# Performance work log

Hardware: AMD Instinct MI355X
Metric: run time of the kernel (lower is better)

Reference implementation:

```python
import jax, jax.numpy as jnp
import numpy as np
from jax import lax

S = 9      # patch feature size (3x3 flattened)
HID = 15   # MI-net hidden width
B = 4096
IMG = 192
PAD = 6


def _linear_params(k, fin, fout):
    bound = 1.0 / np.sqrt(fin)
    kw, kb = jax.random.split(k)
    w = jax.random.uniform(kw, (fout, fin), minval=-bound, maxval=bound, dtype=jnp.float32)
    b = jax.random.uniform(kb, (fout,), minval=-bound, maxval=bound, dtype=jnp.float32)
    return w, b


def setup_inputs() -> dict:
    key = jax.random.key(0)
    ks = jax.random.split(key, 12)
    x = jax.random.normal(ks[0], (B, 1, IMG, IMG), dtype=jnp.float32)
    hc = IMG // 3  # conv output side (stride-3 valid conv)
    ij = jax.random.randint(ks[1], (B, 2), 0, hc, dtype=jnp.int32)
    perm = jax.random.permutation(ks[2], B).astype(jnp.int32)
    cb = 1.0 / np.sqrt(1 * 3 * 3)
    conv_w = jax.random.uniform(ks[3], (1, 1, 3, 3), minval=-cb, maxval=cb, dtype=jnp.float32)
    conv_b = jax.random.uniform(ks[4], (1,), minval=-cb, maxval=cb, dtype=jnp.float32)
    xw1, xb1 = _linear_params(ks[5], S, S)
    xw2, xb2 = _linear_params(ks[6], S, S)
    xw3, xb3 = _linear_params(ks[7], S, HID)
    yw1, yb1 = _linear_params(ks[8], S, S)
    yw2, yb2 = _linear_params(ks[9], S, S)
    yw3, yb3 = _linear_params(ks[10], S, HID)
    fw, fb = _linear_params(ks[11], HID, 1)
    return dict(x=x, ij=ij, perm=perm, conv_w=conv_w, conv_b=conv_b,
                xw1=xw1, xb1=xb1, xw2=xw2, xb2=xb2, xw3=xw3, xb3=xb3,
                yw1=yw1, yb1=yb1, yw2=yw2, yb2=yb2, yw3=yw3, yb3=yb3,
                fw=fw, fb=fb)


def _mi_net(p1, p2, xw1, xb1, xw2, xb2, xw3, xb3,
            yw1, yb1, yw2, yb2, yw3, yb3, fw, fb):
    ix = p1 + jax.nn.relu(p1 @ xw1.T + xb1)
    ix = ix + jax.nn.relu(ix @ xw2.T + xb2)
    ix = ix @ xw3.T + xb3
    iy = p2 + jax.nn.relu(p2 @ yw1.T + yb1)
    iy = iy + jax.nn.relu(iy @ yw2.T + yb2)
    iy = iy @ yw3.T + yb3
    h1 = jax.nn.relu(ix + iy)
    return h1 @ fw.T + fb  # [B, 1]


def reference(x, ij, perm, conv_w, conv_b,
              xw1, xb1, xw2, xb2, xw3, xb3,
              yw1, yb1, yw2, yb2, yw3, yb3, fw, fb):
    # stride-3 valid conv: [B,1,IMG,IMG] -> [B,1,64,64]
    co = lax.conv_general_dilated(x, conv_w, (3, 3), 'VALID',
                                  dimension_numbers=('NCHW', 'OIHW', 'NCHW'))
    co = co[:, 0] + conv_b[0]  # [B, Hc, Wc]
    bn, hc, wc = co.shape
    # pad_circular(data, 6)[i:i+3, j:j+6] == data[(i-6+r) % Hc, (j-6+c) % Wc]
    rows = (ij[:, 0:1] - PAD + jnp.arange(3, dtype=jnp.int32)) % hc  # [B,3]
    cols = (ij[:, 1:2] - PAD + jnp.arange(6, dtype=jnp.int32)) % wc  # [B,6]
    rect = co[jnp.arange(bn)[:, None, None], rows[:, :, None], cols[:, None, :]]  # [B,3,6]
    patch1 = rect[:, :, :3].reshape(-1, S)
    patch2 = rect[:, :, 3:].reshape(-1, S)
    patch2_sh = patch2[perm]
    pred_xy = _mi_net(patch1, patch2, xw1, xb1, xw2, xb2, xw3, xb3,
                      yw1, yb1, yw2, yb2, yw3, yb3, fw, fb)
    pred_x_y = _mi_net(patch1, patch2_sh, xw1, xb1, xw2, xb2, xw3, xb3,
                       yw1, yb1, yw2, yb2, yw3, yb3, fw, fb)
    ret = jnp.mean(pred_xy) - jnp.log(jnp.mean(jnp.exp(pred_x_y)))
    return -ret
```

## Files before the change

### kernel.cpp

```cpp
#include <hip/hip_runtime.h>
#include <math.h>

#define BATCH 4096
#define IMGD 192
#define HC 64
#define PADV 6
#define NBLK 64
#define ITEMS 64

__device__ __forceinline__ void branch9(const float* __restrict__ s, int off,
                                        const float* __restrict__ p, float* __restrict__ out)
{
    float v[9];
    #pragma unroll
    for (int j = 0; j < 9; ++j) {
        float a = s[off + 81 + j];
        #pragma unroll
        for (int k = 0; k < 9; ++k) a += p[k] * s[off + j * 9 + k];
        v[j] = p[j] + fmaxf(a, 0.0f);
    }
    float u[9];
    #pragma unroll
    for (int j = 0; j < 9; ++j) {
        float a = s[off + 171 + j];
        #pragma unroll
        for (int k = 0; k < 9; ++k) a += v[k] * s[off + 90 + j * 9 + k];
        u[j] = v[j] + fmaxf(a, 0.0f);
    }
    #pragma unroll
    for (int j = 0; j < 15; ++j) {
        float a = s[off + 315 + j];
        #pragma unroll
        for (int k = 0; k < 9; ++k) a += u[k] * s[off + 180 + j * 9 + k];
        out[j] = a;
    }
}

__global__ __launch_bounds__(256) void k_fused(
    const float* __restrict__ x, const int* __restrict__ ij,
    const int* __restrict__ perm,
    const float* __restrict__ cw, const float* __restrict__ cb,
    const float* __restrict__ xw1, const float* __restrict__ xb1,
    const float* __restrict__ xw2, const float* __restrict__ xb2,
    const float* __restrict__ xw3, const float* __restrict__ xb3,
    const float* __restrict__ yw1, const float* __restrict__ yb1,
    const float* __restrict__ yw2, const float* __restrict__ yb2,
    const float* __restrict__ yw3, const float* __restrict__ yb3,
    const float* __restrict__ fw, const float* __restrict__ fb,
    float* __restrict__ partials)
{
    __shared__ float s[676];
    __shared__ float lpatch[ITEMS * 27];
    __shared__ float bout[192 * 15];

    int t = threadIdx.x;

    for (int i = t; i < 81; i += 256)  { s[i] = xw1[i];        s[330 + i] = yw1[i];
                                         s[90 + i] = xw2[i];   s[420 + i] = yw2[i]; }
    for (int i = t; i < 135; i += 256) { s[180 + i] = xw3[i];  s[510 + i] = yw3[i]; }
    if (t < 9)  { s[81 + t] = xb1[t];   s[171 + t] = xb2[t];
                  s[411 + t] = yb1[t];  s[501 + t] = yb2[t]; }
    if (t < 15) { s[315 + t] = xb3[t];  s[645 + t] = yb3[t];  s[660 + t] = fw[t]; }
    if (t == 0) s[675] = fb[0];

    float w[9];
    #pragma unroll
    for (int i = 0; i < 9; ++i) w[i] = cw[i];
    float cbias = cb[0];

    int b0 = blockIdx.x * ITEMS;

    for (int idx = t; idx < ITEMS * 27; idx += 256) {
        int item = idx / 27;
        int p    = idx - item * 27;
        int bb, r, c, slot;
        if (p < 18) {
            bb = b0 + item;
            r = p / 6;  c = p - r * 6;
            int half = (c >= 3) ? 1 : 0;
            slot = half * 9 + r * 3 + (c - 3 * half);
        } else {
            int q = p - 18;
            bb = perm[b0 + item];
            r = q / 3;  c = 3 + (q - r * 3);
            slot = 18 + q;
        }
        int i0 = ij[2 * bb], j0 = ij[2 * bb + 1];
        int rr = i0 - PADV + r;  if (rr < 0) rr += HC;
        int cc = j0 - PADV + c;  if (cc < 0) cc += HC;
        const float* xp = x + (size_t)bb * (IMGD * IMGD)
                            + (size_t)(rr * 3) * IMGD + cc * 3;
        float v = cbias;
        v += xp[0]          * w[0] + xp[1]            * w[1] + xp[2]            * w[2];
        v += xp[IMGD]       * w[3] + xp[IMGD + 1]     * w[4] + xp[IMGD + 2]     * w[5];
        v += xp[2 * IMGD]   * w[6] + xp[2 * IMGD + 1] * w[7] + xp[2 * IMGD + 2] * w[8];
        lpatch[item * 27 + slot] = v;
    }
    __syncthreads();

    if (t < 192) {
        int item   = t & 63;
        int branch = t >> 6;
        int woff   = (branch == 0) ? 0 : 330;
        int pbase  = item * 27 + branch * 9;
        float p[9];
        #pragma unroll
        for (int k = 0; k < 9; ++k) p[k] = lpatch[pbase + k];
        float o[15];
        branch9(s, woff, p, o);
        #pragma unroll
        for (int j = 0; j < 15; ++j) bout[t * 15 + j] = o[j];
    }
    __syncthreads();

    if (t < 64) {
        float fbv = s[675];
        float pxy = fbv, pxs = fbv;
        #pragma unroll
        for (int j = 0; j < 15; ++j) {
            float oxj  = bout[t * 15 + j];
            float oyj  = bout[(64 + t) * 15 + j];
            float oysj = bout[(128 + t) * 15 + j];
            float fwj  = s[660 + j];
            pxy += fmaxf(oxj + oyj,  0.0f) * fwj;
            pxs += fmaxf(oxj + oysj, 0.0f) * fwj;
        }
        float e = expf(pxs);
        #pragma unroll
        for (int o = 32; o > 0; o >>= 1) {
            pxy += __shfl_down(pxy, o);
            e   += __shfl_down(e, o);
        }
        if (t == 0) {
            partials[blockIdx.x]        = pxy;
            partials[NBLK + blockIdx.x] = e;
        }
    }
}

__global__ __launch_bounds__(64) void k_final(const float* __restrict__ partials,
                                              float* __restrict__ out)
{
    int t = threadIdx.x;
    float sx = partials[t];
    float se = partials[NBLK + t];
    #pragma unroll
    for (int o = 32; o > 0; o >>= 1) {
        sx += __shfl_down(sx, o);
        se += __shfl_down(se, o);
    }
    if (t == 0) out[0] = logf(se / (float)BATCH) - sx / (float)BATCH;
}

extern "C" void kernel_launch(void* const* d_in, const int* in_sizes, int n_in,
                              void* d_out, int out_size, void* d_ws, size_t ws_size,
                              hipStream_t stream)
{
    const float* x    = (const float*)d_in[0];
    const int*   ij   = (const int*)d_in[1];
    const int*   perm = (const int*)d_in[2];
    const float* cw   = (const float*)d_in[3];
    const float* cb   = (const float*)d_in[4];
    const float* xw1  = (const float*)d_in[5];
    const float* xb1  = (const float*)d_in[6];
    const float* xw2  = (const float*)d_in[7];
    const float* xb2  = (const float*)d_in[8];
    const float* xw3  = (const float*)d_in[9];
    const float* xb3  = (const float*)d_in[10];
    const float* yw1  = (const float*)d_in[11];
    const float* yb1  = (const float*)d_in[12];
    const float* yw2  = (const float*)d_in[13];
    const float* yb2  = (const float*)d_in[14];
    const float* yw3  = (const float*)d_in[15];
    const float* yb3  = (const float*)d_in[16];
    const float* fw   = (const float*)d_in[17];
    const float* fb   = (const float*)d_in[18];

    float* partials = (float*)d_ws;

    k_fused<<<NBLK, 256, 0, stream>>>(x, ij, perm, cw, cb,
                                      xw1, xb1, xw2, xb2, xw3, xb3,
                                      yw1, yb1, yw2, yb2, yw3, yb3,
                                      fw, fb, partials);
    k_final<<<1, 64, 0, stream>>>(partials, (float*)d_out);
}
```

Before: 14.57 us.

## Spread batch over 256 blocks of 16 items and stage perm/ij indices in LDS

Raises the grid from 64 to 256 blocks, each handling 16 batch items instead of 64, so more CUs on the GPU get work. The perm and ij lookups are loaded once per item into shared memory in two dependent stages, so the dependent global reads no longer repeat per patch element. The final reduction kernel now combines 256 partials across four wavefronts. The cost is two extra block barriers, and only 48 of 256 threads run the MLP stage.

```diff
diff --git a/kernel.cpp b/kernel.cpp
--- a/kernel.cpp
+++ b/kernel.cpp
@@ -5,8 +5,8 @@
 #define IMGD 192
 #define HC 64
 #define PADV 6
-#define NBLK 64
-#define ITEMS 64
+#define NBLK2 256
+#define IPB 16
 
 __device__ __forceinline__ void branch9(const float* __restrict__ s, int off,
                                         const float* __restrict__ p, float* __restrict__ out)
@@ -50,10 +50,13 @@
     float* __restrict__ partials)
 {
     __shared__ float s[676];
-    __shared__ float lpatch[ITEMS * 27];
-    __shared__ float bout[192 * 15];
-
-    int t = threadIdx.x;
+    __shared__ int   pidx[IPB];
+    __shared__ int   ij4[IPB * 4];
+    __shared__ float lpatch[IPB * 27];
+    __shared__ float bout[48 * 15];
+
+    int t  = threadIdx.x;
+    int b0 = blockIdx.x * IPB;
 
     for (int i = t; i < 81; i += 256)  { s[i] = xw1[i];        s[330 + i] = yw1[i];
                                          s[90 + i] = xw2[i];   s[420 + i] = yw2[i]; }
@@ -68,24 +71,32 @@
     for (int i = 0; i < 9; ++i) w[i] = cw[i];
     float cbias = cb[0];
 
-    int b0 = blockIdx.x * ITEMS;
-
-    for (int idx = t; idx < ITEMS * 27; idx += 256) {
+    if (t < IPB) pidx[t] = perm[b0 + t];
+    __syncthreads();
+    if (t < 2 * IPB) {
+        int item = t & (IPB - 1);
+        int sel  = t >> 4;
+        int bb   = sel ? pidx[item] : (b0 + item);
+        ij4[item * 4 + sel * 2 + 0] = ij[2 * bb];
+        ij4[item * 4 + sel * 2 + 1] = ij[2 * bb + 1];
+    }
+    __syncthreads();
+
+    for (int idx = t; idx < IPB * 27; idx += 256) {
         int item = idx / 27;
         int p    = idx - item * 27;
-        int bb, r, c, slot;
+        int r, c, sel, slot;
         if (p < 18) {
-            bb = b0 + item;
-            r = p / 6;  c = p - r * 6;
+            r = p / 6;  c = p - r * 6;  sel = 0;
             int half = (c >= 3) ? 1 : 0;
             slot = half * 9 + r * 3 + (c - 3 * half);
         } else {
             int q = p - 18;
-            bb = perm[b0 + item];
-            r = q / 3;  c = 3 + (q - r * 3);
+            r = q / 3;  c = 3 + (q - r * 3);  sel = 1;
             slot = 18 + q;
         }
-        int i0 = ij[2 * bb], j0 = ij[2 * bb + 1];
+        int bb = sel ? pidx[item] : (b0 + item);
+        int i0 = ij4[item * 4 + sel * 2], j0 = ij4[item * 4 + sel * 2 + 1];
         int rr = i0 - PADV + r;  if (rr < 0) rr += HC;
         int cc = j0 - PADV + c;  if (cc < 0) cc += HC;
         const float* xp = x + (size_t)bb * (IMGD * IMGD)
@@ -98,9 +109,9 @@
     }
     __syncthreads();
 
-    if (t < 192) {
-        int item   = t & 63;
-        int branch = t >> 6;
+    if (t < 48) {
+        int item   = t & 15;
+        int branch = t >> 4;
         int woff   = (branch == 0) ? 0 : 330;
         int pbase  = item * 27 + branch * 9;
         float p[9];
@@ -113,43 +124,51 @@
     }
     __syncthreads();
 
-    if (t < 64) {
+    if (t < IPB) {
         float fbv = s[675];
         float pxy = fbv, pxs = fbv;
         #pragma unroll
         for (int j = 0; j < 15; ++j) {
             float oxj  = bout[t * 15 + j];
-            float oyj  = bout[(64 + t) * 15 + j];
-            float oysj = bout[(128 + t) * 15 + j];
+            float oyj  = bout[(16 + t) * 15 + j];
+            float oysj = bout[(32 + t) * 15 + j];
             float fwj  = s[660 + j];
             pxy += fmaxf(oxj + oyj,  0.0f) * fwj;
             pxs += fmaxf(oxj + oysj, 0.0f) * fwj;
         }
         float e = expf(pxs);
         #pragma unroll
-        for (int o = 32; o > 0; o >>= 1) {
+        for (int o = 8; o > 0; o >>= 1) {
             pxy += __shfl_down(pxy, o);
             e   += __shfl_down(e, o);
         }
         if (t == 0) {
-            partials[blockIdx.x]        = pxy;
-            partials[NBLK + blockIdx.x] = e;
-        }
-    }
-}
-
-__global__ __launch_bounds__(64) void k_final(const float* __restrict__ partials,
-                                              float* __restrict__ out)
-{
+            partials[blockIdx.x]         = pxy;
+            partials[NBLK2 + blockIdx.x] = e;
+        }
+    }
+}
+
+__global__ __launch_bounds__(256) void k_final(const float* __restrict__ partials,
+                                               float* __restrict__ out)
+{
+    __shared__ float r1[4], r2[4];
     int t = threadIdx.x;
     float sx = partials[t];
-    float se = partials[NBLK + t];
+    float se = partials[NBLK2 + t];
     #pragma unroll
     for (int o = 32; o > 0; o >>= 1) {
         sx += __shfl_down(sx, o);
         se += __shfl_down(se, o);
     }
-    if (t == 0) out[0] = logf(se / (float)BATCH) - sx / (float)BATCH;
+    int wid = t >> 6, lane = t & 63;
+    if (lane == 0) { r1[wid] = sx; r2[wid] = se; }
+    __syncthreads();
+    if (t == 0) {
+        float S  = (r1[0] + r1[1]) + (r1[2] + r1[3]);
+        float E  = (r2[0] + r2[1]) + (r2[2] + r2[3]);
+        out[0] = logf(E / (float)BATCH) - S / (float)BATCH;
+    }
 }
 
 extern "C" void kernel_launch(void* const* d_in, const int* in_sizes, int n_in,
@@ -178,9 +197,9 @@
 
     float* partials = (float*)d_ws;
 
-    k_fused<<<NBLK, 256, 0, stream>>>(x, ij, perm, cw, cb,
-                                      xw1, xb1, xw2, xb2, xw3, xb3,
-                                      yw1, yb1, yw2, yb2, yw3, yb3,
-                                      fw, fb, partials);
-    k_final<<<1, 64, 0, stream>>>(partials, (float*)d_out);
-}
+    k_fused<<<NBLK2, 256, 0, stream>>>(x, ij, perm, cw, cb,
+                                       xw1, xb1, xw2, xb2, xw3, xb3,
+                                       yw1, yb1, yw2, yb2, yw3, yb3,
+                                       fw, fb, partials);
+    k_final<<<1, 256, 0, stream>>>(partials, (float*)d_out);
+}
```

Result: faster. 12.38 us (-15.0%).
